# Optimization experiments

Hardware: AMD Instinct MI355X
Metric: run time of the kernel (lower is better)

Reference implementation:

```python
import jax, jax.numpy as jnp
import numpy as np

B, S, H = 1, 4096, 2048
HQ, HKV, D = 8, 4, 256
WIN = 1024          # sliding window
SOFTCAP = 50.0      # attn logit softcapping
EPS = 1e-6          # rms_norm_eps
ROPE_THETA = 10000.0


def setup_inputs() -> dict:
    key = jax.random.key(0)
    ks = jax.random.split(key, 6)
    hidden_states = jax.random.normal(ks[0], (B, S, H), dtype=jnp.float32)
    # RoPE cos/sin tables, shape [B, S, D]
    inv_freq = 1.0 / (ROPE_THETA ** (jnp.arange(0, D, 2, dtype=jnp.float32) / D))
    pos = jnp.arange(S, dtype=jnp.float32)
    freqs = pos[:, None] * inv_freq[None, :]          # [S, D/2]
    emb = jnp.concatenate([freqs, freqs], axis=-1)    # [S, D]
    cos = jnp.broadcast_to(jnp.cos(emb)[None], (B, S, D)).astype(jnp.float32)
    sin = jnp.broadcast_to(jnp.sin(emb)[None], (B, S, D)).astype(jnp.float32)
    qpos = jnp.arange(S)[:, None]
    kpos = jnp.arange(S)[None, :]
    diff = qpos - kpos
    allowed = (diff >= 0) & (diff < WIN)
    attention_mask = jnp.where(allowed, 0.0, -1e9).astype(jnp.float32)[None, None]
    attention_mask = jnp.broadcast_to(attention_mask, (B, 1, S, S))
    w_scale = 0.02
    Wq = jax.random.normal(ks[1], (HQ * D, H), dtype=jnp.float32) * w_scale
    Wk = jax.random.normal(ks[2], (HKV * D, H), dtype=jnp.float32) * w_scale
    Wv = jax.random.normal(ks[3], (HKV * D, H), dtype=jnp.float32) * w_scale
    Wo = jax.random.normal(ks[4], (H, HQ * D), dtype=jnp.float32) * w_scale
    q_norm_w = jnp.ones((D,), dtype=jnp.float32)
    k_norm_w = jnp.ones((D,), dtype=jnp.float32)
    return {"hidden_states": hidden_states, "cos": cos, "sin": sin,
            "attention_mask": attention_mask, "Wq": Wq, "Wk": Wk, "Wv": Wv,
            "Wo": Wo, "q_norm_w": q_norm_w, "k_norm_w": k_norm_w}


def _rms_norm(x, weight=None):
    # Gemma4 RMSNorm in fp32: x * rsqrt(mean(x^2) + eps) [* weight]
    ms = jnp.mean(x * x, axis=-1, keepdims=True) + EPS
    y = x * jax.lax.rsqrt(ms)
    return y * weight if weight is not None else y


def _rope(x, cos, sin):
    # x: [B,S,Hn,D]; cos/sin: [B,S,D] -> unsqueeze at dim 2
    x1, x2 = jnp.split(x, 2, axis=-1)
    rot = jnp.concatenate([-x2, x1], axis=-1)
    return x * cos[:, :, None, :] + rot * sin[:, :, None, :]


def reference(hidden_states, cos, sin, attention_mask, Wq, Wk, Wv, Wo, q_norm_w, k_norm_w):
    n_rep = HQ // HKV
    q = (hidden_states @ Wq.T).reshape(B, S, HQ, D)     # [B,S,HQ,D]
    q = _rms_norm(q, q_norm_w)
    q = _rope(q, cos, sin).transpose(0, 2, 1, 3)        # [B,HQ,S,D]
    k = (hidden_states @ Wk.T).reshape(B, S, HKV, D)
    k = _rms_norm(k, k_norm_w)
    k = _rope(k, cos, sin).transpose(0, 2, 1, 3)        # [B,HKV,S,D]
    v = (hidden_states @ Wv.T).reshape(B, S, HKV, D)
    v = _rms_norm(v).transpose(0, 2, 1, 3)              # [B,HKV,S,D]
    # repeat_kv (GQA)
    k = jnp.repeat(k, n_rep, axis=1)                    # [B,HQ,S,D]
    v = jnp.repeat(v, n_rep, axis=1)
    scores = jnp.einsum('bhqd,bhkd->bhqk', q, k)        # scaling = 1.0
    scores = jnp.tanh(scores / SOFTCAP) * SOFTCAP       # softcap
    scores = scores + attention_mask
    attn = jax.nn.softmax(scores.astype(jnp.float32), axis=-1).astype(q.dtype)
    out = jnp.einsum('bhqk,bhkd->bhqd', attn, v)        # [B,HQ,S,D]
    out = out.transpose(0, 2, 1, 3).reshape(B, S, HQ * D)
    return out @ Wo.T                                   # [B,S,H]
```

## Files before the change

kernel.cpp:

```cpp
#include <hip/hip_runtime.h>

#define S_LEN 4096
#define HID   2048
#define NHQ   8
#define NKV   4
#define DHEAD 256
#define WIN   1024

typedef __attribute__((ext_vector_type(4))) float     floatx4;
typedef __attribute__((ext_vector_type(8))) _Float16  halfx8;
typedef __attribute__((ext_vector_type(8))) __bf16    bf16x8;

__device__ __forceinline__ unsigned short f2h(float f){
  union { _Float16 h; unsigned short u; } cv; cv.h = (_Float16)f; return cv.u;
}
__device__ __forceinline__ float h2f(unsigned short u){
  union { unsigned short u; _Float16 h; } cv; cv.u = u; return (float)cv.h;
}
__device__ __forceinline__ unsigned short f2bf(float f){
  unsigned int u = __float_as_uint(f);
  u += 0x7FFFu + ((u >> 16) & 1u);
  return (unsigned short)(u >> 16);
}

__device__ __forceinline__ void gld_lds16(const void* g, void* l){
  __builtin_amdgcn_global_load_lds((const __attribute__((address_space(1))) void*)g,
                                   (__attribute__((address_space(3))) void*)l, 16, 0, 0);
}

__global__ __launch_bounds__(256) void cvt_all(const float* __restrict__ hs,
                                               const float* __restrict__ Wq,
                                               const float* __restrict__ Wk,
                                               const float* __restrict__ Wv,
                                               const float* __restrict__ Wo,
                                               unsigned short* __restrict__ h_h,
                                               unsigned short* __restrict__ w_qkv,
                                               unsigned short* __restrict__ wo){
  int bid = blockIdx.x;
  const float* src;
  unsigned short* dst;
  size_t i;
  if (bid < 8192){
    i = ((size_t)bid * 256 + threadIdx.x) * 4;
    src = hs + i; dst = h_h + i;
  } else if (bid < 16384){
    i = ((size_t)(bid - 8192) * 256 + threadIdx.x) * 4;
    int row = (int)(i >> 11), col = (int)(i & 2047);
    src = ((row < 2048) ? (Wq + ((size_t)row << 11))
         : (row < 3072) ? (Wk + ((size_t)(row - 2048) << 11))
                        : (Wv + ((size_t)(row - 3072) << 11))) + col;
    dst = w_qkv + i;
  } else {
    i = ((size_t)(bid - 16384) * 256 + threadIdx.x) * 4;
    src = Wo + i; dst = wo + i;
  }
  float4 v = *(const float4*)src;
  *(ushort4*)dst = make_ushort4(f2h(v.x), f2h(v.y), f2h(v.z), f2h(v.w));
}

template<int OUT_F32>
__global__ __launch_bounds__(512, 2) void gemm_qkv8(const unsigned short* __restrict__ A,
                                                    const unsigned short* __restrict__ B,
                                                    void* __restrict__ Cv,
                                                    int ldC, int K, int nx){
  __shared__ __align__(16) unsigned short As[2][256 * 64];
  __shared__ __align__(16) unsigned short Bs[2][256 * 64];
  const int T = K >> 6;
  const int t0 = threadIdx.x, w = t0 >> 6, lane = t0 & 63;
  const int wm = w >> 2, wn = w & 3;
  const int quad = lane >> 4, l15 = lane & 15;
  const int r7 = l15 & 7;

  const int bid = (int)blockIdx.x;
  const int by = bid / nx, bx = bid - by * nx;
  const int bm0 = by * 256, bn0 = bx * 256;

  const int grow = lane >> 3;
  const int sg8  = (((lane & 7) ^ grow) << 3);

#define STGH(U, HALF)                                                          \
  {                                                                            \
    const int sl_ = (U) & 1;                                                   \
    const unsigned short* src_ = ((HALF) < 2)                                  \
        ? (A + (size_t)(bm0 + (((HALF) & 1) << 7)) * K)                        \
        : (B + (size_t)(bn0 + (((HALF) & 1) << 7)) * K);                       \
    unsigned short* dst_ = (((HALF) < 2) ? &As[sl_][0] : &Bs[sl_][0])          \
                           + ((((HALF) & 1) << 7) * 64);                       \
    _Pragma("unroll")                                                          \
    for (int L = 0; L < 2; ++L){                                               \
      const int ck = L * 8 + w;                                                \
      gld_lds16(src_ + (size_t)((ck << 3) + grow) * K + (size_t)(U) * 64 + sg8,\
                dst_ + ck * 512);                                              \
    }                                                                          \
  }

#define LDA(MI, KS) (*(const halfx8*)&Ap[(wm*128 + (MI)*16 + l15) * 64 + ((((KS)*4 + quad) ^ r7) << 3)])
#define LDB(NI, KS) (*(const halfx8*)&Bp[(wn*64  + (NI)*16 + l15) * 64 + ((((KS)*4 + quad) ^ r7) << 3)])

  STGH(0, 0) STGH(0, 1) STGH(0, 2) STGH(0, 3)
  asm volatile("s_waitcnt vmcnt(0)" ::: "memory");
  __builtin_amdgcn_s_barrier();

  const floatx4 zf = {0.f, 0.f, 0.f, 0.f};
  floatx4 acc[8][4];
#pragma unroll
  for (int mi = 0; mi < 8; ++mi)
#pragma unroll
    for (int ni = 0; ni < 4; ++ni) acc[mi][ni] = zf;

  for (int t = 0; t < T; ++t){
    const int cur = t & 1;
    const unsigned short* Ap = &As[cur][0];
    const unsigned short* Bp = &Bs[cur][0];
    const bool pf = (t + 1 < T);
    halfx8 af[4], bf0[4], bf1[4];

#pragma unroll
    for (int mi = 0; mi < 4; ++mi) af[mi] = LDA(mi, 0);
#pragma unroll
    for (int ni = 0; ni < 4; ++ni){ bf0[ni] = LDB(ni, 0); bf1[ni] = LDB(ni, 1); }
    if (pf) STGH(t + 1, 0)
    __builtin_amdgcn_s_barrier();
    asm volatile("s_waitcnt lgkmcnt(0)" ::: "memory");
    __builtin_amdgcn_sched_barrier(0);
    __builtin_amdgcn_s_setprio(1);
#pragma unroll
    for (int mi = 0; mi < 4; ++mi)
#pragma unroll
      for (int ni = 0; ni < 4; ++ni)
        acc[mi][ni] = __builtin_amdgcn_mfma_f32_16x16x32_f16(af[mi], bf0[ni], acc[mi][ni], 0, 0, 0);
    __builtin_amdgcn_s_setprio(0);
    __builtin_amdgcn_s_barrier();
    __builtin_amdgcn_sched_barrier(0);

#pragma unroll
    for (int mi = 0; mi < 4; ++mi) af[mi] = LDA(4 + mi, 0);
    if (pf) STGH(t + 1, 1)
    __builtin_amdgcn_s_barrier();
    asm volatile("s_waitcnt lgkmcnt(0)" ::: "memory");
    __builtin_amdgcn_sched_barrier(0);
    __builtin_amdgcn_s_setprio(1);
#pragma unroll
    for (int mi = 0; mi < 4; ++mi)
#pragma unroll
      for (int ni = 0; ni < 4; ++ni)
        acc[4 + mi][ni] = __builtin_amdgcn_mfma_f32_16x16x32_f16(af[mi], bf0[ni], acc[4 + mi][ni], 0, 0, 0);
    __builtin_amdgcn_s_setprio(0);
    __builtin_amdgcn_s_barrier();
    __builtin_amdgcn_sched_barrier(0);

#pragma unroll
    for (int mi = 0; mi < 4; ++mi) af[mi] = LDA(mi, 1);
    if (pf) STGH(t + 1, 2)
    __builtin_amdgcn_s_barrier();
    asm volatile("s_waitcnt lgkmcnt(0)" ::: "memory");
    __builtin_amdgcn_sched_barrier(0);
    __builtin_amdgcn_s_setprio(1);
#pragma unroll
    for (int mi = 0; mi < 4; ++mi)
#pragma unroll
      for (int ni = 0; ni < 4; ++ni)
        acc[mi][ni] = __builtin_amdgcn_mfma_f32_16x16x32_f16(af[mi], bf1[ni], acc[mi][ni], 0, 0, 0);
    __builtin_amdgcn_s_setprio(0);
    __builtin_amdgcn_s_barrier();
    __builtin_amdgcn_sched_barrier(0);

#pragma unroll
    for (int mi = 0; mi < 4; ++mi) af[mi] = LDA(4 + mi, 1);
    if (pf) STGH(t + 1, 3)
    __builtin_amdgcn_s_barrier();
    asm volatile("s_waitcnt lgkmcnt(0)" ::: "memory");
    __builtin_amdgcn_sched_barrier(0);
    __builtin_amdgcn_s_setprio(1);
#pragma unroll
    for (int mi = 0; mi < 4; ++mi)
#pragma unroll
      for (int ni = 0; ni < 4; ++ni)
        acc[4 + mi][ni] = __builtin_amdgcn_mfma_f32_16x16x32_f16(af[mi], bf1[ni], acc[4 + mi][ni], 0, 0, 0);
    __builtin_amdgcn_s_setprio(0);
    if (pf) { asm volatile("s_waitcnt vmcnt(0)" ::: "memory"); }
    __builtin_amdgcn_s_barrier();
    __builtin_amdgcn_sched_barrier(0);
  }
#undef STGH
#undef LDA
#undef LDB

#pragma unroll
  for (int mi = 0; mi < 8; ++mi)
#pragma unroll
    for (int ni = 0; ni < 4; ++ni)
#pragma unroll
      for (int r = 0; r < 4; ++r){
        int m = bm0 + wm*128 + mi*16 + quad*4 + r;
        int n = bn0 + wn*64 + ni*16 + l15;
        float v = acc[mi][ni][r];
        if (OUT_F32) ((float*)Cv)[(size_t)m * ldC + n] = v;
        else         ((unsigned short*)Cv)[(size_t)m * ldC + n] = f2h(v);
      }
}

__global__ __launch_bounds__(256) void qkv_post(const unsigned short* __restrict__ qkvh,
                                                const float* __restrict__ cosb,
                                                const float* __restrict__ sinb,
                                                const float* __restrict__ qnw,
                                                const float* __restrict__ knw,
                                                unsigned short* __restrict__ Qf,
                                                unsigned short* __restrict__ Kf,
                                                unsigned short* __restrict__ Vf){
  int gw   = blockIdx.x * 4 + (threadIdx.x >> 6);
  int lane = threadIdx.x & 63;
  int hh = gw & 15, s = gw >> 4;
  int colbase = (hh < 8) ? hh * 256 : (hh < 12 ? 2048 + (hh - 8) * 256 : 3072 + (hh - 12) * 256);

  ushort4 raw = *(const ushort4*)(qkvh + (size_t)s * 4096 + colbase + lane * 4);
  float x0 = h2f(raw.x), x1 = h2f(raw.y), x2 = h2f(raw.z), x3 = h2f(raw.w);
  float ss = x0*x0 + x1*x1 + x2*x2 + x3*x3;
#pragma unroll
  for (int off = 32; off; off >>= 1) ss += __shfl_xor(ss, off);
  float inv = rsqrtf(ss * (1.0f / 256.0f) + 1e-6f);

  if (hh < 12){
    const float* wp = (hh < 8) ? qnw : knw;
    float4 wv = *(const float4*)(wp + lane * 4);
    float y[4] = { x0*inv*wv.x, x1*inv*wv.y, x2*inv*wv.z, x3*inv*wv.w };
    float4 cv = *(const float4*)(cosb + (size_t)s * 256 + lane * 4);
    float4 sv = *(const float4*)(sinb + (size_t)s * 256 + lane * 4);
    float cj[4] = {cv.x, cv.y, cv.z, cv.w};
    float sj[4] = {sv.x, sv.y, sv.z, sv.w};
    unsigned short oh[4];
#pragma unroll
    for (int j = 0; j < 4; ++j){
      float oth = __shfl_xor(y[j], 32);
      float rot = (lane < 32) ? -oth : oth;
      oh[j] = f2h(y[j] * cj[j] + rot * sj[j]);
    }
    ushort4 r = make_ushort4(oh[0], oh[1], oh[2], oh[3]);
    if (hh < 8) *(ushort4*)(Qf + (size_t)(hh       * S_LEN + s) * DHEAD + lane * 4) = r;
    else        *(ushort4*)(Kf + (size_t)((hh - 8) * S_LEN + s) * DHEAD + lane * 4) = r;
  } else {
    ushort4 r = make_ushort4(f2bf(x0*inv), f2bf(x1*inv), f2bf(x2*inv), f2bf(x3*inv));
    *(ushort4*)(Vf + (size_t)((hh - 12) * S_LEN + s) * DHEAD + lane * 4) = r;
  }
}

__global__ __launch_bounds__(256) void transpose_v(const unsigned short* __restrict__ v,
                                                   unsigned short* __restrict__ vt){
  __shared__ unsigned short tile[64][68];
  int kv = blockIdx.z, d0 = blockIdx.x * 64, s0 = blockIdx.y * 64;
  int t = threadIdx.x;
  int r = t >> 4, c4 = (t & 15) * 4;
#pragma unroll
  for (int i = 0; i < 4; ++i){
    int row = r + i * 16;
    ushort4 xx = *(const ushort4*)(v + (size_t)(kv * S_LEN + s0 + row) * DHEAD + d0 + c4);
    tile[row][c4] = xx.x; tile[row][c4+1] = xx.y; tile[row][c4+2] = xx.z; tile[row][c4+3] = xx.w;
  }
  __syncthreads();
#pragma unroll
  for (int i = 0; i < 4; ++i){
    int dr = r + i * 16;
    ushort4 yy = make_ushort4(tile[c4][dr], tile[c4+1][dr], tile[c4+2][dr], tile[c4+3][dr]);
    *(ushort4*)(vt + (size_t)(kv * DHEAD + d0 + dr) * S_LEN + s0 + c4) = yy;
  }
}

__global__ __launch_bounds__(512, 2) void attn_win(const unsigned short* __restrict__ Qg,
                                                   const unsigned short* __restrict__ Kg,
                                                   const unsigned short* __restrict__ Vt,
                                                   unsigned short* __restrict__ Og){
  __shared__ __align__(16) unsigned short Ks[2][8 * 32 * 32];
  __shared__ __align__(16) unsigned short Vts[2][256 * 32];
  __shared__ __align__(16) unsigned short Pb[8][16 * 40];

  const int bid = blockIdx.x;
  const int h = bid & 7, kv = h >> 1;
  const int q0 = (bid >> 3) * 128;
  const int t = threadIdx.x, w = t >> 6, lane = t & 63;
  const int quad = lane >> 4, l15 = lane & 15;
  const int l2 = lane >> 2;
  const int gsw = (((lane & 3) ^ ((l2 >> 1) & 3)) << 3);
  const int qsw = ((quad ^ ((l15 >> 1) & 3)) << 3);
  const int qw0 = q0 + w * 16;

  halfx8 qf[8];
#pragma unroll
  for (int c = 0; c < 8; ++c)
    qf[c] = *(const halfx8*)(Qg + (size_t)(h * S_LEN + qw0 + l15) * DHEAD + c*32 + quad*8);

  const floatx4 zf = {0.f, 0.f, 0.f, 0.f};
  floatx4 oacc[16];
#pragma unroll
  for (int dt = 0; dt < 16; ++dt) oacc[dt] = zf;
  float l_part[4] = {0.f, 0.f, 0.f, 0.f};

  int kt_lo = q0 / 32 - 32; if (kt_lo < 0) kt_lo = 0;
  int kt_hi = q0 / 32 + 3;

  const size_t kbase = (size_t)kv * S_LEN * DHEAD;
  const size_t vbase = (size_t)kv * DHEAD * S_LEN;

#define STAGE(KT, B)                                                              \
  {                                                                               \
    const int key0_ = (KT) * 32;                                                  \
    _Pragma("unroll")                                                             \
    for (int j = 0; j < 2; ++j){                                                  \
      int ch = j * 8 + w;                                                         \
      int krow = (ch & 1) * 16 + l2;                                              \
      int cb = ch >> 1;                                                           \
      gld_lds16(Kg + kbase + (size_t)(key0_ + krow) * DHEAD + cb * 32 + gsw,      \
                &Ks[B][ch * 512]);                                                \
      int drow = ch * 16 + l2;                                                    \
      gld_lds16(Vt + vbase + (size_t)drow * S_LEN + key0_ + gsw,                  \
                &Vts[B][ch * 512]);                                               \
    }                                                                             \
  }

  STAGE(kt_lo, 0);

  for (int kt = kt_lo; kt <= kt_hi; ++kt){
    const int cur = (kt - kt_lo) & 1;
    if (kt < kt_hi){
      STAGE(kt + 1, cur ^ 1);
      asm volatile("s_waitcnt vmcnt(4)" ::: "memory");
    } else {
      asm volatile("s_waitcnt vmcnt(0)" ::: "memory");
    }
    __builtin_amdgcn_s_barrier();

    const int key0 = kt * 32;
    if (key0 <= qw0 + 15 && key0 + 31 >= qw0 - (WIN - 1)){
      floatx4 sc[2];
      sc[0] = zf; sc[1] = zf;
      __builtin_amdgcn_s_setprio(1);
#pragma unroll
      for (int c = 0; c < 8; ++c){
#pragma unroll
        for (int nt = 0; nt < 2; ++nt){
          halfx8 kf = *(const halfx8*)&Ks[cur][c * 1024 + (nt*16 + l15) * 32 + qsw];
          sc[nt] = __builtin_amdgcn_mfma_f32_16x16x32_f16(qf[c], kf, sc[nt], 0, 0, 0);
        }
      }
      __builtin_amdgcn_s_setprio(0);
      const bool tfull = (key0 + 31 <= qw0) && (qw0 + 15 - key0 < WIN);
#pragma unroll
      for (int nt = 0; nt < 2; ++nt)
#pragma unroll
        for (int r = 0; r < 4; ++r){
          float v = sc[nt][r];
          float e  = __builtin_amdgcn_exp2f(v * 0.0577078016f);
          float tt = __builtin_amdgcn_rcpf(e + 1.0f);
          float p  = __builtin_amdgcn_exp2f(fmaf(tt, -144.26950408f, 28.8539008f));
          if (!tfull){
            int qi = qw0 + quad*4 + r;
            int ki = key0 + nt*16 + l15;
            p = ((ki <= qi) && (qi - ki < WIN)) ? p : 0.0f;
          }
          l_part[r] += p;
          Pb[w][(quad*4 + r) * 40 + nt*16 + l15] = f2bf(p);
        }
      bf16x8 pf = *(const bf16x8*)&Pb[w][l15 * 40 + quad * 8];
      __builtin_amdgcn_s_setprio(1);
#pragma unroll
      for (int dt = 0; dt < 16; ++dt){
        bf16x8 vf = *(const bf16x8*)&Vts[cur][(dt*16 + l15) * 32 + qsw];
        oacc[dt] = __builtin_amdgcn_mfma_f32_16x16x32_bf16(pf, vf, oacc[dt], 0, 0, 0);
      }
      __builtin_amdgcn_s_setprio(0);
    }
    __builtin_amdgcn_s_barrier();
  }
#undef STAGE

#pragma unroll
  for (int r = 0; r < 4; ++r){
    float l = l_part[r];
    l += __shfl_xor(l, 1);
    l += __shfl_xor(l, 2);
    l += __shfl_xor(l, 4);
    l += __shfl_xor(l, 8);
    float rl = 1.0f / l;
    int srow = qw0 + quad*4 + r;
#pragma unroll
    for (int dt = 0; dt < 16; ++dt)
      Og[(size_t)srow * (NHQ * DHEAD) + h * DHEAD + dt*16 + l15] = f2h(oacc[dt][r] * rl);
  }
}

extern "C" void kernel_launch(void* const* d_in, const int* in_sizes, int n_in,
                              void* d_out, int out_size, void* d_ws, size_t ws_size,
                              hipStream_t stream){
  const float* hs   = (const float*)d_in[0];
  const float* cosb = (const float*)d_in[1];
  const float* sinb = (const float*)d_in[2];
  const float* Wq   = (const float*)d_in[4];
  const float* Wk   = (const float*)d_in[5];
  const float* Wv   = (const float*)d_in[6];
  const float* Wo   = (const float*)d_in[7];
  const float* qnw  = (const float*)d_in[8];
  const float* knw  = (const float*)d_in[9];
  float* out = (float*)d_out;

  const size_t MB = 1024ull * 1024ull;
  char* ws = (char*)d_ws;
  unsigned short* h_h   = (unsigned short*)(ws);
  unsigned short* w_qkv = (unsigned short*)(ws + 16 * MB);
  unsigned short* wo    = (unsigned short*)(ws + 32 * MB);
  unsigned short* qkvh  = (unsigned short*)(ws + 40 * MB);
  unsigned short* Qf    = (unsigned short*)(ws);
  unsigned short* Kf    = (unsigned short*)(ws + 16 * MB);
  unsigned short* Vf    = (unsigned short*)(ws + 24 * MB);
  unsigned short* vt    = (unsigned short*)(ws + 40 * MB);
  unsigned short* ob    = (unsigned short*)(ws + 48 * MB);

  cvt_all<<<20480, 256, 0, stream>>>(hs, Wq, Wk, Wv, Wo, h_h, w_qkv, wo);

  gemm_qkv8<0><<<256, 512, 0, stream>>>(h_h, w_qkv, qkvh, 4096, 2048, 16);

  qkv_post<<<16384, 256, 0, stream>>>(qkvh, cosb, sinb, qnw, knw, Qf, Kf, Vf);
  transpose_v<<<dim3(4, 64, 4), 256, 0, stream>>>(Vf, vt);

  attn_win<<<256, 512, 0, stream>>>(Qf, Kf, vt, ob);

  gemm_qkv8<1><<<128, 512, 0, stream>>>(ob, wo, out, 2048, 2048, 8);
}
```

Measured before the change: 398.1 us.

## Give each attention wave two 16-row query subtiles to reuse K/V fragments

The windowed attention kernel now runs 4 waves per block instead of 8, and each wave handles 32 query rows as two 16-row subtiles. Each K and V fragment read from LDS now feeds two MFMAs, halving LDS fragment traffic per unit of compute, and each thread issues more staging loads per tile. The cost is doubled accumulator and Q-fragment registers (launch bounds set to 256 threads, 1 block), fewer waves to hide latency, and coarser tile-skip decisions at the 32-row granularity.

Result: slower. 431.0 us (+8.3%).

```diff
diff --git a/kernel.cpp b/kernel.cpp
--- a/kernel.cpp
+++ b/kernel.cpp
@@ -265,13 +265,13 @@
   }
 }
 
-__global__ __launch_bounds__(512, 2) void attn_win(const unsigned short* __restrict__ Qg,
+__global__ __launch_bounds__(256, 1) void attn_win(const unsigned short* __restrict__ Qg,
                                                    const unsigned short* __restrict__ Kg,
                                                    const unsigned short* __restrict__ Vt,
                                                    unsigned short* __restrict__ Og){
   __shared__ __align__(16) unsigned short Ks[2][8 * 32 * 32];
   __shared__ __align__(16) unsigned short Vts[2][256 * 32];
-  __shared__ __align__(16) unsigned short Pb[8][16 * 40];
+  __shared__ __align__(16) unsigned short Pb[4][32 * 40];
 
   const int bid = blockIdx.x;
   const int h = bid & 7, kv = h >> 1;
@@ -281,18 +281,22 @@
   const int l2 = lane >> 2;
   const int gsw = (((lane & 3) ^ ((l2 >> 1) & 3)) << 3);
   const int qsw = ((quad ^ ((l15 >> 1) & 3)) << 3);
-  const int qw0 = q0 + w * 16;
-
-  halfx8 qf[8];
-#pragma unroll
-  for (int c = 0; c < 8; ++c)
-    qf[c] = *(const halfx8*)(Qg + (size_t)(h * S_LEN + qw0 + l15) * DHEAD + c*32 + quad*8);
+  const int qw0 = q0 + w * 32;
+
+  halfx8 qf[2][8];
+#pragma unroll
+  for (int s = 0; s < 2; ++s)
+#pragma unroll
+    for (int c = 0; c < 8; ++c)
+      qf[s][c] = *(const halfx8*)(Qg + (size_t)(h * S_LEN + qw0 + s*16 + l15) * DHEAD + c*32 + quad*8);
 
   const floatx4 zf = {0.f, 0.f, 0.f, 0.f};
-  floatx4 oacc[16];
-#pragma unroll
-  for (int dt = 0; dt < 16; ++dt) oacc[dt] = zf;
-  float l_part[4] = {0.f, 0.f, 0.f, 0.f};
+  floatx4 oacc[2][16];
+#pragma unroll
+  for (int s = 0; s < 2; ++s)
+#pragma unroll
+    for (int dt = 0; dt < 16; ++dt) oacc[s][dt] = zf;
+  float l_part[2][4] = {{0.f,0.f,0.f,0.f},{0.f,0.f,0.f,0.f}};
 
   int kt_lo = q0 / 32 - 32; if (kt_lo < 0) kt_lo = 0;
   int kt_hi = q0 / 32 + 3;
@@ -304,8 +308,8 @@
   {                                                                               \
     const int key0_ = (KT) * 32;                                                  \
     _Pragma("unroll")                                                             \
-    for (int j = 0; j < 2; ++j){                                                  \
-      int ch = j * 8 + w;                                                         \
+    for (int j = 0; j < 4; ++j){                                                  \
+      int ch = j * 4 + w;                                                         \
       int krow = (ch & 1) * 16 + l2;                                              \
       int cb = ch >> 1;                                                           \
       gld_lds16(Kg + kbase + (size_t)(key0_ + krow) * DHEAD + cb * 32 + gsw,      \
@@ -322,49 +326,54 @@
     const int cur = (kt - kt_lo) & 1;
     if (kt < kt_hi){
       STAGE(kt + 1, cur ^ 1);
-      asm volatile("s_waitcnt vmcnt(4)" ::: "memory");
+      asm volatile("s_waitcnt vmcnt(8)" ::: "memory");
     } else {
       asm volatile("s_waitcnt vmcnt(0)" ::: "memory");
     }
     __builtin_amdgcn_s_barrier();
 
     const int key0 = kt * 32;
-    if (key0 <= qw0 + 15 && key0 + 31 >= qw0 - (WIN - 1)){
-      floatx4 sc[2];
-      sc[0] = zf; sc[1] = zf;
+    if (key0 <= qw0 + 31 && key0 + 31 >= qw0 - (WIN - 1)){
+      floatx4 sc[2][2];
+      sc[0][0] = zf; sc[0][1] = zf; sc[1][0] = zf; sc[1][1] = zf;
       __builtin_amdgcn_s_setprio(1);
 #pragma unroll
       for (int c = 0; c < 8; ++c){
 #pragma unroll
         for (int nt = 0; nt < 2; ++nt){
           halfx8 kf = *(const halfx8*)&Ks[cur][c * 1024 + (nt*16 + l15) * 32 + qsw];
-          sc[nt] = __builtin_amdgcn_mfma_f32_16x16x32_f16(qf[c], kf, sc[nt], 0, 0, 0);
+          sc[0][nt] = __builtin_amdgcn_mfma_f32_16x16x32_f16(qf[0][c], kf, sc[0][nt], 0, 0, 0);
+          sc[1][nt] = __builtin_amdgcn_mfma_f32_16x16x32_f16(qf[1][c], kf, sc[1][nt], 0, 0, 0);
         }
       }
       __builtin_amdgcn_s_setprio(0);
-      const bool tfull = (key0 + 31 <= qw0) && (qw0 + 15 - key0 < WIN);
-#pragma unroll
-      for (int nt = 0; nt < 2; ++nt)
-#pragma unroll
-        for (int r = 0; r < 4; ++r){
-          float v = sc[nt][r];
-          float e  = __builtin_amdgcn_exp2f(v * 0.0577078016f);
-          float tt = __builtin_amdgcn_rcpf(e + 1.0f);
-          float p  = __builtin_amdgcn_exp2f(fmaf(tt, -144.26950408f, 28.8539008f));
-          if (!tfull){
-            int qi = qw0 + quad*4 + r;
-            int ki = key0 + nt*16 + l15;
-            p = ((ki <= qi) && (qi - ki < WIN)) ? p : 0.0f;
+      const bool tfull = (key0 + 31 <= qw0) && (qw0 + 31 - key0 < WIN);
+#pragma unroll
+      for (int s = 0; s < 2; ++s)
+#pragma unroll
+        for (int nt = 0; nt < 2; ++nt)
+#pragma unroll
+          for (int r = 0; r < 4; ++r){
+            float v = sc[s][nt][r];
+            float e  = __builtin_amdgcn_exp2f(v * 0.0577078016f);
+            float tt = __builtin_amdgcn_rcpf(e + 1.0f);
+            float p  = __builtin_amdgcn_exp2f(fmaf(tt, -144.26950408f, 28.8539008f));
+            if (!tfull){
+              int qi = qw0 + s*16 + quad*4 + r;
+              int ki = key0 + nt*16 + l15;
+              p = ((ki <= qi) && (qi - ki < WIN)) ? p : 0.0f;
+            }
+            l_part[s][r] += p;
+            Pb[w][(s*16 + quad*4 + r) * 40 + nt*16 + l15] = f2bf(p);
           }
-          l_part[r] += p;
-          Pb[w][(quad*4 + r) * 40 + nt*16 + l15] = f2bf(p);
-        }
-      bf16x8 pf = *(const bf16x8*)&Pb[w][l15 * 40 + quad * 8];
+      bf16x8 pf0 = *(const bf16x8*)&Pb[w][l15 * 40 + quad * 8];
+      bf16x8 pf1 = *(const bf16x8*)&Pb[w][(16 + l15) * 40 + quad * 8];
       __builtin_amdgcn_s_setprio(1);
 #pragma unroll
       for (int dt = 0; dt < 16; ++dt){
         bf16x8 vf = *(const bf16x8*)&Vts[cur][(dt*16 + l15) * 32 + qsw];
-        oacc[dt] = __builtin_amdgcn_mfma_f32_16x16x32_bf16(pf, vf, oacc[dt], 0, 0, 0);
+        oacc[0][dt] = __builtin_amdgcn_mfma_f32_16x16x32_bf16(pf0, vf, oacc[0][dt], 0, 0, 0);
+        oacc[1][dt] = __builtin_amdgcn_mfma_f32_16x16x32_bf16(pf1, vf, oacc[1][dt], 0, 0, 0);
       }
       __builtin_amdgcn_s_setprio(0);
     }
@@ -373,18 +382,20 @@
 #undef STAGE
 
 #pragma unroll
-  for (int r = 0; r < 4; ++r){
-    float l = l_part[r];
-    l += __shfl_xor(l, 1);
-    l += __shfl_xor(l, 2);
-    l += __shfl_xor(l, 4);
-    l += __shfl_xor(l, 8);
-    float rl = 1.0f / l;
-    int srow = qw0 + quad*4 + r;
-#pragma unroll
-    for (int dt = 0; dt < 16; ++dt)
-      Og[(size_t)srow * (NHQ * DHEAD) + h * DHEAD + dt*16 + l15] = f2h(oacc[dt][r] * rl);
-  }
+  for (int s = 0; s < 2; ++s)
+#pragma unroll
+    for (int r = 0; r < 4; ++r){
+      float l = l_part[s][r];
+      l += __shfl_xor(l, 1);
+      l += __shfl_xor(l, 2);
+      l += __shfl_xor(l, 4);
+      l += __shfl_xor(l, 8);
+      float rl = 1.0f / l;
+      int srow = qw0 + s*16 + quad*4 + r;
+#pragma unroll
+      for (int dt = 0; dt < 16; ++dt)
+        Og[(size_t)srow * (NHQ * DHEAD) + h * DHEAD + dt*16 + l15] = f2h(oacc[s][dt][r] * rl);
+    }
 }
 
 extern "C" void kernel_launch(void* const* d_in, const int* in_sizes, int n_in,
@@ -420,7 +431,7 @@
   qkv_post<<<16384, 256, 0, stream>>>(qkvh, cosb, sinb, qnw, knw, Qf, Kf, Vf);
   transpose_v<<<dim3(4, 64, 4), 256, 0, stream>>>(Vf, vt);
 
-  attn_win<<<256, 512, 0, stream>>>(Qf, Kf, vt, ob);
+  attn_win<<<256, 256, 0, stream>>>(Qf, Kf, vt, ob);
 
   gemm_qkv8<1><<<128, 512, 0, stream>>>(ob, wo, out, 2048, 2048, 8);
 }
```

## Double key tile to 64 per iteration in windowed attention kernel

Applied to the files above, without the earlier changes.

Raises the attention key tile from 32 to 64 keys per loop step, halving the number of barrier-separated iterations and staging larger K/V chunks with a new XOR swizzle for the transposed V tile. Each iteration now issues twice as many score and PV MFMAs between barriers. Shared memory per block doubles (about 148 KB), so launch bounds drop to one 512-thread block per CU, trading occupancy for less sync overhead. Masked edge tiles also grow, wasting some compute at window boundaries.

Result: faster. 390.3 us (-2.0%).

```diff
diff --git a/kernel.cpp b/kernel.cpp
--- a/kernel.cpp
+++ b/kernel.cpp
@@ -265,13 +265,13 @@
   }
 }
 
-__global__ __launch_bounds__(512, 2) void attn_win(const unsigned short* __restrict__ Qg,
+__global__ __launch_bounds__(512, 1) void attn_win(const unsigned short* __restrict__ Qg,
                                                    const unsigned short* __restrict__ Kg,
                                                    const unsigned short* __restrict__ Vt,
                                                    unsigned short* __restrict__ Og){
-  __shared__ __align__(16) unsigned short Ks[2][8 * 32 * 32];
-  __shared__ __align__(16) unsigned short Vts[2][256 * 32];
-  __shared__ __align__(16) unsigned short Pb[8][16 * 40];
+  __shared__ __align__(16) unsigned short Ks[2][2 * 8192];
+  __shared__ __align__(16) unsigned short Vts[2][256 * 64];
+  __shared__ __align__(16) unsigned short Pb[8][16 * 72];
 
   const int bid = blockIdx.x;
   const int h = bid & 7, kv = h >> 1;
@@ -280,6 +280,7 @@
   const int quad = lane >> 4, l15 = lane & 15;
   const int l2 = lane >> 2;
   const int gsw = (((lane & 3) ^ ((l2 >> 1) & 3)) << 3);
+  const int sgv = (((lane & 7) ^ ((lane >> 3) & 7)) << 3);
   const int qsw = ((quad ^ ((l15 >> 1) & 3)) << 3);
   const int qw0 = q0 + w * 16;
 
@@ -294,24 +295,26 @@
   for (int dt = 0; dt < 16; ++dt) oacc[dt] = zf;
   float l_part[4] = {0.f, 0.f, 0.f, 0.f};
 
-  int kt_lo = q0 / 32 - 32; if (kt_lo < 0) kt_lo = 0;
-  int kt_hi = q0 / 32 + 3;
+  int kt_lo = q0 / 64 - 16; if (kt_lo < 0) kt_lo = 0;
+  int kt_hi = q0 / 64 + 1;
 
   const size_t kbase = (size_t)kv * S_LEN * DHEAD;
   const size_t vbase = (size_t)kv * DHEAD * S_LEN;
 
 #define STAGE(KT, B)                                                              \
   {                                                                               \
-    const int key0_ = (KT) * 32;                                                  \
+    const int key0_ = (KT) * 64;                                                  \
     _Pragma("unroll")                                                             \
-    for (int j = 0; j < 2; ++j){                                                  \
-      int ch = j * 8 + w;                                                         \
-      int krow = (ch & 1) * 16 + l2;                                              \
-      int cb = ch >> 1;                                                           \
+    for (int j = 0; j < 4; ++j){                                                  \
+      int ch  = j * 8 + w;                                             \
+      int chl = ch & 15;                                                          \
+      int sk  = ch >> 4;                                                          \
+      int krow = sk * 32 + (chl & 1) * 16 + l2;                                   \
+      int cb = chl >> 1;                                                          \
       gld_lds16(Kg + kbase + (size_t)(key0_ + krow) * DHEAD + cb * 32 + gsw,      \
-                &Ks[B][ch * 512]);                                                \
-      int drow = ch * 16 + l2;                                                    \
-      gld_lds16(Vt + vbase + (size_t)drow * S_LEN + key0_ + gsw,                  \
+                &Ks[B][sk * 8192 + chl * 512]);                                   \
+      int drow = ch * 8 + (lane >> 3);                                            \
+      gld_lds16(Vt + vbase + (size_t)drow * S_LEN + key0_ + sgv,                  \
                 &Vts[B][ch * 512]);                                               \
     }                                                                             \
   }
@@ -322,29 +325,30 @@
     const int cur = (kt - kt_lo) & 1;
     if (kt < kt_hi){
       STAGE(kt + 1, cur ^ 1);
-      asm volatile("s_waitcnt vmcnt(4)" ::: "memory");
+      asm volatile("s_waitcnt vmcnt(8)" ::: "memory");
     } else {
       asm volatile("s_waitcnt vmcnt(0)" ::: "memory");
     }
     __builtin_amdgcn_s_barrier();
 
-    const int key0 = kt * 32;
-    if (key0 <= qw0 + 15 && key0 + 31 >= qw0 - (WIN - 1)){
-      floatx4 sc[2];
-      sc[0] = zf; sc[1] = zf;
+    const int key0 = kt * 64;
+    if (key0 <= qw0 + 15 && key0 + 63 >= qw0 - (WIN - 1)){
+      floatx4 sc[4];
+      sc[0] = zf; sc[1] = zf; sc[2] = zf; sc[3] = zf;
       __builtin_amdgcn_s_setprio(1);
 #pragma unroll
       for (int c = 0; c < 8; ++c){
 #pragma unroll
-        for (int nt = 0; nt < 2; ++nt){
-          halfx8 kf = *(const halfx8*)&Ks[cur][c * 1024 + (nt*16 + l15) * 32 + qsw];
+        for (int nt = 0; nt < 4; ++nt){
+          halfx8 kf = *(const halfx8*)&Ks[cur][(nt >> 1) * 8192 + c * 1024
+                                               + ((nt & 1) * 16 + l15) * 32 + qsw];
           sc[nt] = __builtin_amdgcn_mfma_f32_16x16x32_f16(qf[c], kf, sc[nt], 0, 0, 0);
         }
       }
       __builtin_amdgcn_s_setprio(0);
-      const bool tfull = (key0 + 31 <= qw0) && (qw0 + 15 - key0 < WIN);
-#pragma unroll
-      for (int nt = 0; nt < 2; ++nt)
+      const bool tfull = (key0 + 63 <= qw0) && (qw0 + 15 - key0 < WIN);
+#pragma unroll
+      for (int nt = 0; nt < 4; ++nt)
 #pragma unroll
         for (int r = 0; r < 4; ++r){
           float v = sc[nt][r];
@@ -357,14 +361,18 @@
             p = ((ki <= qi) && (qi - ki < WIN)) ? p : 0.0f;
           }
           l_part[r] += p;
-          Pb[w][(quad*4 + r) * 40 + nt*16 + l15] = f2bf(p);
+          Pb[w][(quad*4 + r) * 72 + nt*16 + l15] = f2bf(p);
         }
-      bf16x8 pf = *(const bf16x8*)&Pb[w][l15 * 40 + quad * 8];
+      bf16x8 pf0 = *(const bf16x8*)&Pb[w][l15 * 72 + quad * 8];
+      bf16x8 pf1 = *(const bf16x8*)&Pb[w][l15 * 72 + 32 + quad * 8];
       __builtin_amdgcn_s_setprio(1);
 #pragma unroll
       for (int dt = 0; dt < 16; ++dt){
-        bf16x8 vf = *(const bf16x8*)&Vts[cur][(dt*16 + l15) * 32 + qsw];
-        oacc[dt] = __builtin_amdgcn_mfma_f32_16x16x32_bf16(pf, vf, oacc[dt], 0, 0, 0);
+        const int r = dt*16 + l15;
+        bf16x8 vf0 = *(const bf16x8*)&Vts[cur][r * 64 + ((quad       ^ (r & 7)) << 3)];
+        bf16x8 vf1 = *(const bf16x8*)&Vts[cur][r * 64 + (((4 + quad) ^ (r & 7)) << 3)];
+        oacc[dt] = __builtin_amdgcn_mfma_f32_16x16x32_bf16(pf0, vf0, oacc[dt], 0, 0, 0);
+        oacc[dt] = __builtin_amdgcn_mfma_f32_16x16x32_bf16(pf1, vf1, oacc[dt], 0, 0, 0);
       }
       __builtin_amdgcn_s_setprio(0);
     }
```
